# Kernel optimization log

Hardware: AMD Instinct MI355X
Metric: run time of the kernel (lower is better)

## Reference

```python
import jax, jax.numpy as jnp
import numpy as np

EPS = 1e-12  # F.normalize eps


def setup_inputs() -> dict:
    key = jax.random.key(0)
    ks = jax.random.split(key, 6)
    B, T, D = 8, 4096, 1024
    L, K, CD = 8, 1024, 16
    return {
        "z_e": jax.random.normal(ks[0], (B, T, D), jnp.float32),
        "Wd": jax.random.normal(ks[1], (L, CD, D), jnp.float32) * 0.02,
        "bd": jnp.zeros((L, CD), jnp.float32),
        "cb": jax.random.normal(ks[2], (L, K, CD), jnp.float32) * 0.02,
        "Wu": jax.random.normal(ks[3], (L, D, CD), jnp.float32) * 0.02,
        "bu": jnp.zeros((L, D), jnp.float32),
    }


def _l2norm(x):
    return x / jnp.maximum(jnp.linalg.norm(x, axis=-1, keepdims=True), EPS)


def reference(z_e, Wd, bd, cb, Wu, bu):
    """z_e: (B,T,D). Returns (z_q_concat, codes, commitment_loss, codebook_loss, entropy_loss)."""
    B, T, D = z_e.shape
    L, K, CD = cb.shape
    sg = jax.lax.stop_gradient
    residual = z_e
    zq_list, codes_list = [], []
    commit = jnp.asarray(0.0, z_e.dtype)
    cbl = jnp.asarray(0.0, z_e.dtype)
    for i in range(L):
        # proj_down: Linear(D -> CD), weight (CD, D)
        z_i = jnp.einsum('btd,cd->btc', residual, Wd[i]) + bd[i]  # (B,T,CD)
        flat = z_i.reshape(-1, CD)                                 # (N,CD)
        cb_i = cb[i]                                               # (K,CD)
        # L2-normalized lookup; argmin of euclidean cdist == argmin of squared dist
        zn, cbn = _l2norm(flat), _l2norm(cb_i)
        d2 = (jnp.sum(zn * zn, -1, keepdims=True)
              - 2.0 * (zn @ cbn.T)
              + jnp.sum(cbn * cbn, -1))                            # (N,K)
        codes = jnp.argmin(d2, axis=-1)                            # (N,)
        z_q = cb_i[codes].reshape(B, T, CD)                        # gather from RAW codebook
        commit = commit + jnp.mean((z_i - sg(z_q)) ** 2)
        cbl = cbl + jnp.mean((z_q - sg(z_i)) ** 2)
        zq_list.append(z_i + sg(z_q - z_i))                        # straight-through
        # residual update uses detached z_q; proj_up weight (D, CD)
        residual = residual - (jnp.einsum('btc,dc->btd', sg(z_q), Wu[i]) + bu[i])
        codes_list.append(codes.reshape(B, T))
    z_q_concat = jnp.concatenate(zq_list, axis=-1)                 # (B,T,L*CD)
    codes_all = jnp.stack(codes_list, axis=-1)                     # (B,T,L)
    entropy_loss = jnp.asarray(0.0, z_e.dtype)                     # entropy_loss_weight == 0
    return z_q_concat, codes_all, commit, cbl, entropy_loss
```

## Files before the change

### kernel.cpp

```cpp
#include <hip/hip_runtime.h>
#include <math.h>


#define TAU 3e-4f

#define WS_WACC   0
#define WS_HV64   64
#define WS_G64    2048
#define WS_CBN64  133120
#define WS_CBF    1247232
#define WS_G32    1902592
#define WS_HV32   1968128
#define WS_BF     1968640
#define BF_LO_OFF 131072

typedef __attribute__((ext_vector_type(8))) short short8v;
typedef __attribute__((ext_vector_type(4))) float f32x4;

__device__ __forceinline__ unsigned short bf16_rne(float x) {
    unsigned u = __float_as_uint(x);
    u += 0x7FFFu + ((u >> 16) & 1u);
    return (unsigned short)(u >> 16);
}
__device__ __forceinline__ float bf16_to_f32(unsigned short h) {
    return __uint_as_float(((unsigned)h) << 16);
}

__global__ void __launch_bounds__(256) rvq_prep(
    const float* __restrict__ cb, const float* __restrict__ Wd,
    const float* __restrict__ Wu, const float* __restrict__ bd,
    const float* __restrict__ bu,
    double* __restrict__ cbn64, unsigned short* __restrict__ cbf,
    unsigned short* __restrict__ Bf,
    double* __restrict__ G64, float* __restrict__ G32,
    double* __restrict__ hv64, float* __restrict__ hv32,
    double* __restrict__ wacc)
{
    __shared__ double sm2[1200];
    float* smf = (float*)sm2;
    const int b = blockIdx.x, t = threadIdx.x;
    if (b < 32) {
        const int idx = b * 256 + t;
        const float* cp = cb + (size_t)idx * 16;
        double v[16]; double n = 0.0;
#pragma unroll
        for (int c = 0; c < 16; ++c) { v[c] = (double)cp[c]; n = fma(v[c], v[c], n); }
        const double iv = 1.0 / fmax(sqrt(n), 1e-12);
        double* r64 = cbn64 + (size_t)idx * 17;
        unsigned short* cf = cbf + (size_t)idx * 32;
        double c2 = 0.0;
#pragma unroll
        for (int c = 0; c < 16; ++c) {
            const double x = v[c] * iv;
            c2 = fma(x, x, c2);
            r64[c] = x;
            const float xf = (float)x;
            const unsigned short hh = bf16_rne(xf);
            cf[c] = hh;
            cf[16 + c] = bf16_rne(xf - bf16_to_f32(hh));
        }
        r64[16] = c2;
    } else if (b < 96) {
        const int u = (b - 32) * 4 + (t >> 6);
        const int lane = t & 63;
        const int ks = u >> 3, ctg = u & 7;
        const int ic = ctg * 16 + (lane & 15);
        const int kb = ks * 32 + (lane >> 4) * 8;
        const float* wp = Wd + (size_t)ic * 1024 + kb;
        const float4 w0 = *(const float4*)wp;
        const float4 w1 = *(const float4*)(wp + 4);
        const float wv[8] = {w0.x, w0.y, w0.z, w0.w, w1.x, w1.y, w1.z, w1.w};
        unsigned short* dst = Bf + ((size_t)(ks * 8 + ctg) * 64 + lane) * 8;
#pragma unroll
        for (int i = 0; i < 8; ++i) {
            const unsigned short hh = bf16_rne(wv[i]);
            dst[i] = hh;
            dst[BF_LO_OFF + i] = bf16_rne(wv[i] - bf16_to_f32(hh));
        }
    } else if (b < 160) {
        const int j = (b - 96) >> 3, i = (b - 96) & 7;
        if (j >= i) return;
        float* Aus = smf;
        float* Bds = smf + 1280;
        const int a = t >> 4, bb = t & 15;
        double s = 0.0;
        for (int ch = 0; ch < 16; ++ch) {
            __syncthreads();
            {
                const int dd = t >> 2, a4 = (t & 3) * 4;
                const float4 v = *(const float4*)(Wu + (size_t)j * 16384
                                  + (size_t)(ch * 64 + dd) * 16 + a4);
                *(float4*)&Aus[dd * 20 + a4] = v;
                const int br = t >> 4, d4 = (t & 15) * 4;
                const float4 w = *(const float4*)(Wd + (size_t)i * 16384
                                  + (size_t)br * 1024 + ch * 64 + d4);
                *(float4*)&Bds[br * 68 + d4] = w;
            }
            __syncthreads();
#pragma unroll
            for (int dd = 0; dd < 64; ++dd)
                s = fma((double)Aus[dd * 20 + a], (double)Bds[bb * 68 + dd], s);
        }
        G64[(size_t)(j * 8 + i) * 256 + t] = s;
        G32[(size_t)(j * 8 + i) * 256 + t] = (float)s;
    } else if (b < 168) {
        const int i = b - 160;
        const int dq = t >> 4, bb = t & 15;
        const float* wp = Wd + (size_t)i * 16384 + (size_t)bb * 1024 + dq * 64;
        const float* bup = bu + dq * 64;
        double s = 0.0;
        for (int dd = 0; dd < 64; ++dd) {
            double sb = 0.0;
            for (int j = 0; j < i; ++j) sb += (double)bup[j * 1024 + dd];
            s = fma(sb, (double)wp[dd], s);
        }
        sm2[dq * 20 + bb] = s;
        __syncthreads();
        if (t < 16) {
            double s2 = 0.0;
#pragma unroll
            for (int q = 0; q < 16; ++q) s2 += sm2[q * 20 + t];
            const double h = (double)bd[i * 16 + t] - s2;
            hv64[i * 16 + t] = h; hv32[i * 16 + t] = (float)h;
        }
    } else {
        if (t == 0) wacc[0] = 0.0;
    }
}

__global__ void __launch_bounds__(256, 4) rvq_main(
    const float* __restrict__ z_e, const float* __restrict__ Wd,
    const float* __restrict__ cb,
    const unsigned short* __restrict__ Bf, const float* __restrict__ hv32,
    const double* __restrict__ hv64,
    const unsigned short* __restrict__ cbf, const double* __restrict__ cbn64,
    const float* __restrict__ G32, const double* __restrict__ G64,
    double* __restrict__ wacc,
    float* __restrict__ out0, float* __restrict__ out1)
{
    __shared__ __attribute__((aligned(16))) double stag_d[896];
    __shared__ float ybuf[32 * 132];
    __shared__ float candd[128], candd2[128];
    __shared__ int   candk[128];
    __shared__ float zqs[32 * 17];
    __shared__ int   bkhist[256];
    __shared__ int   bks[32], flist[32];
    __shared__ int   flagcnt;
    float* stag = reinterpret_cast<float*>(stag_d);

    const int t = threadIdx.x;
    const int tok0g = blockIdx.x * 32;
    const int wq = t >> 6, lane = t & 63;
    const int blk = lane >> 4, col = lane & 15, kh = blk & 1;
    const bool lolane = blk >= 2;

    {
        const int Ch = wq >> 1, Tt = wq & 1;
        const float* zrow = z_e + (size_t)(tok0g + Tt * 16 + col) * 1024 + blk * 8;
        const unsigned short* bfh = Bf + ((size_t)(Ch * 4) * 64 + lane) * 8;
        f32x4 acc[4];
#pragma unroll
        for (int ct = 0; ct < 4; ++ct) acc[ct] = (f32x4){0.f, 0.f, 0.f, 0.f};

#pragma unroll 2
        for (int ks = 0; ks < 32; ++ks) {
            const float4 a0 = *(const float4*)(zrow + ks * 32);
            const float4 a1 = *(const float4*)(zrow + ks * 32 + 4);
            const float av[8] = {a0.x, a0.y, a0.z, a0.w, a1.x, a1.y, a1.z, a1.w};
            short8v ah, al;
#pragma unroll
            for (int i = 0; i < 8; ++i) {
                const unsigned short hh = bf16_rne(av[i]);
                ah[i] = (short)hh;
                al[i] = (short)bf16_rne(av[i] - bf16_to_f32(hh));
            }
            const unsigned short* bp = bfh + (size_t)ks * 4096;
#pragma unroll
            for (int ct = 0; ct < 4; ++ct) {
                const short8v bh = *(const short8v*)(bp + ct * 512);
                const short8v bl = *(const short8v*)(bp + BF_LO_OFF + ct * 512);
                acc[ct] = __builtin_amdgcn_mfma_f32_16x16x32_bf16(ah, bh, acc[ct], 0, 0, 0);
                acc[ct] = __builtin_amdgcn_mfma_f32_16x16x32_bf16(ah, bl, acc[ct], 0, 0, 0);
                acc[ct] = __builtin_amdgcn_mfma_f32_16x16x32_bf16(al, bh, acc[ct], 0, 0, 0);
            }
        }
#pragma unroll
        for (int ct = 0; ct < 4; ++ct) {
            const float hvv = hv32[Ch * 64 + ct * 16 + col];
#pragma unroll
            for (int r = 0; r < 4; ++r)
                ybuf[(Tt * 16 + blk * 4 + r) * 132 + Ch * 64 + ct * 16 + col]
                    = acc[ct][r] + hvv;
        }
    }

    double lacc = 0.0;
    const int q = wq;
#pragma unroll 1
    for (int l = 0; l < 8; ++l) {
        __syncthreads();

        short8v af[2];
#pragma unroll
        for (int h = 0; h < 2; ++h) {
            const float* yp = &ybuf[(h * 16 + col) * 132 + l * 16 + kh * 8];
            const float4 y0 = *(const float4*)yp;
            const float4 y1 = *(const float4*)(yp + 4);
            const float yv[8] = {y0.x, y0.y, y0.z, y0.w, y1.x, y1.y, y1.z, y1.w};
            float p = 0.f;
#pragma unroll
            for (int i = 0; i < 8; ++i) p = fmaf(yv[i], yv[i], p);
            const float n2 = p + __shfl_xor(p, 16);
            const float iv = 1.0f / fmaxf(sqrtf(n2), 1e-12f);
#pragma unroll
            for (int i = 0; i < 8; ++i) {
                const float x = -2.f * (yv[i] * iv);
                const unsigned short hh = bf16_rne(x);
                af[h][i] = (short)(lolane ? bf16_rne(x - bf16_to_f32(hh)) : hh);
            }
        }

        float bs[2][4], bs2[2][4]; int bk[2][4];
#pragma unroll
        for (int h = 0; h < 2; ++h)
#pragma unroll
            for (int r = 0; r < 4; ++r) { bs[h][r] = 1e30f; bs2[h][r] = 1e30f; bk[h][r] = -1; }
        const unsigned short* cbp = cbf + ((size_t)(l * 1024 + q * 256 + col)) * 32;
        const unsigned short* p1 = cbp + kh * 8;
        const unsigned short* p2 = cbp + 16 + kh * 8;
#pragma unroll 2
        for (int tile = 0; tile < 16; ++tile) {
            const short8v b1 = *(const short8v*)(p1 + tile * 512);
            short8v b2 = {};
            if (!lolane) b2 = *(const short8v*)(p2 + tile * 512);
            f32x4 aa[2];
            aa[0] = (f32x4){0.f, 0.f, 0.f, 0.f};
            aa[0] = __builtin_amdgcn_mfma_f32_16x16x32_bf16(af[0], b1, aa[0], 0, 0, 0);
            aa[0] = __builtin_amdgcn_mfma_f32_16x16x32_bf16(af[0], b2, aa[0], 0, 0, 0);
            aa[1] = (f32x4){0.f, 0.f, 0.f, 0.f};
            aa[1] = __builtin_amdgcn_mfma_f32_16x16x32_bf16(af[1], b1, aa[1], 0, 0, 0);
            aa[1] = __builtin_amdgcn_mfma_f32_16x16x32_bf16(af[1], b2, aa[1], 0, 0, 0);
            const int k = q * 256 + tile * 16 + col;
#pragma unroll
            for (int h = 0; h < 2; ++h)
#pragma unroll
                for (int r = 0; r < 4; ++r) {
                    const float s = aa[h][r];
                    const bool wn = s < bs[h][r];
                    bs2[h][r] = wn ? bs[h][r] : fminf(bs2[h][r], s);
                    bk[h][r]  = wn ? k : bk[h][r];
                    bs[h][r]  = wn ? s : bs[h][r];
                }
        }

#pragma unroll
        for (int m = 1; m <= 8; m <<= 1)
#pragma unroll
            for (int h = 0; h < 2; ++h)
#pragma unroll
                for (int r = 0; r < 4; ++r) {
                    const float ob = __shfl_xor(bs[h][r], m);
                    const float os = __shfl_xor(bs2[h][r], m);
                    const int   ok = __shfl_xor(bk[h][r], m);
                    const bool wn = (ob < bs[h][r]) || (ob == bs[h][r] && ok < bk[h][r]);
                    const float loser = wn ? bs[h][r] : ob;
                    bs2[h][r] = fminf(fminf(bs2[h][r], os), loser);
                    bs[h][r]  = wn ? ob : bs[h][r];
                    bk[h][r]  = wn ? ok : bk[h][r];
                }
        if (t == 0) flagcnt = 0;
        if (col == 0) {
#pragma unroll
            for (int h = 0; h < 2; ++h)
#pragma unroll
                for (int r = 0; r < 4; ++r) {
                    const int tok = h * 16 + blk * 4 + r;
                    candd [q * 32 + tok] = bs[h][r];
                    candd2[q * 32 + tok] = bs2[h][r];
                    candk [q * 32 + tok] = bk[h][r];
                }
        }
        __syncthreads();
        if (t < 32) {
            float best = 1e30f, sec = 1e30f; int bkk = -1;
#pragma unroll
            for (int c = 0; c < 4; ++c) {
                const float d  = candd [c * 32 + t];
                const float d2 = candd2[c * 32 + t];
                const int   k  = candk [c * 32 + t];
                const bool wn = (d < best) || (d == best && k < bkk);
                const float nw = fminf(sec, fminf(best, d2));
                const float nl = fminf(sec, d);
                sec  = wn ? nw : nl;
                bkk  = wn ? k : bkk;
                best = wn ? d : best;
            }
            bks[t] = bkk;
            const float* yr = &ybuf[t * 132 + l * 16];
            float n2 = 0.f;
#pragma unroll
            for (int c = 0; c < 16; ++c) n2 = fmaf(yr[c], yr[c], n2);
            if ((sec - best < TAU) || (n2 < 1e-3f)) {
                const int p = atomicAdd(&flagcnt, 1); flist[p] = t;
            }
        }
        __syncthreads();

        const int nf = flagcnt;
#pragma unroll 1
        for (int f = 0; f < nf; ++f) {
            const int tok = flist[f];
            double* rpd = stag_d;
            {
                const int c = t & 15, ch = t >> 4;
                const float* gz = z_e + (size_t)(tok0g + tok) * 1024 + ch * 64;
                const float* wp = Wd + ((size_t)l * 16 + c) * 1024 + ch * 64;
                double pd = 0.0;
                for (int dd = 0; dd < 64; ++dd)
                    pd = fma((double)gz[dd], (double)wp[dd], pd);
                rpd[c * 16 + ch] = pd;
            }
            __syncthreads();
            if (t < 16) {
                double y = hv64[l * 16 + t];
#pragma unroll
                for (int ch = 0; ch < 16; ++ch) y += rpd[t * 16 + ch];
                for (int j = 0; j < l; ++j) {
                    const int bkj = bkhist[tok * 8 + j];
                    const float* qv = cb + ((size_t)j * 1024 + bkj) * 16;
                    const double* gp = G64 + (size_t)(j * 8 + l) * 256 + t;
                    double s = 0.0;
#pragma unroll
                    for (int a = 0; a < 16; ++a)
                        s = fma((double)qv[a], gp[a * 16], s);
                    y -= s;
                }
                rpd[256 + t] = y;
            }
            __syncthreads();
            if (t == 0) {
                double n2 = 0.0;
#pragma unroll
                for (int c = 0; c < 16; ++c) n2 = fma(rpd[256 + c], rpd[256 + c], n2);
                const double iv = 1.0 / fmax(sqrt(n2), 1e-12);
#pragma unroll
                for (int c = 0; c < 16; ++c) rpd[272 + c] = rpd[256 + c] * iv;
            }
            __syncthreads();
            {
                double bd_ = 1e300; int bk_ = -1;
#pragma unroll
                for (int qq = 0; qq < 4; ++qq) {
                    const int k = qq * 256 + t;
                    const double* row = cbn64 + (size_t)(l * 1024 + k) * 17;
                    double dot = 0.0;
#pragma unroll
                    for (int c = 0; c < 16; ++c) dot = fma(row[c], rpd[272 + c], dot);
                    const double s = fma(-2.0, dot, row[16]);
                    if (s < bd_) { bd_ = s; bk_ = k; }
                }
                rpd[288 + t] = bd_;
                ((int*)&rpd[544])[t] = bk_;
            }
            __syncthreads();
            if (t == 0) {
                double bd_ = 1e300; int bk_ = -1;
                for (int i = 0; i < 256; ++i) {
                    const double d = rpd[288 + i];
                    const int k = ((int*)&rpd[544])[i];
                    if (d < bd_ || (d == bd_ && k < bk_)) { bd_ = d; bk_ = k; }
                }
                bks[tok] = bk_;
            }
            __syncthreads();
        }

        if (t < 32) {
            const int bk_ = bks[t];
            bkhist[t * 8 + l] = bk_;
            const float4* qp = (const float4*)(cb + ((size_t)l * 1024 + bk_) * 16);
            const float4 q0 = qp[0], q1 = qp[1], q2 = qp[2], q3 = qp[3];
            float* op = out0 + (size_t)(tok0g + t) * 128 + l * 16;
            ((float4*)op)[0] = q0; ((float4*)op)[1] = q1;
            ((float4*)op)[2] = q2; ((float4*)op)[3] = q3;
            out1[(size_t)(tok0g + t) * 8 + l] = (float)bk_;
            const float qf[16] = {q0.x,q0.y,q0.z,q0.w, q1.x,q1.y,q1.z,q1.w,
                                  q2.x,q2.y,q2.z,q2.w, q3.x,q3.y,q3.z,q3.w};
#pragma unroll
            for (int a = 0; a < 16; ++a) zqs[t * 17 + a] = qf[a];
            const float* yr = &ybuf[t * 132 + l * 16];
#pragma unroll
            for (int c = 0; c < 16; ++c) {
                const float d = yr[c] - qf[c];
                lacc += (double)d * (double)d;
            }
        }
        __syncthreads();

        if (l < 7) {
            {
                const int total = (7 - l) * 256;
                for (int idx = t; idx < total; idx += 256) {
                    const int ii = l + 1 + (idx >> 8);
                    stag[idx] = G32[(size_t)(l * 8 + ii) * 256 + (idx & 255)];
                }
            }
            __syncthreads();
            const int part = t >> 5, tok = t & 31;
            const int ii = l + 1 + part;
            if (ii < 8) {
                float zql[16];
#pragma unroll
                for (int a = 0; a < 16; ++a) zql[a] = zqs[tok * 17 + a];
                const float* gb = &stag[part * 256];
                float corr[16];
#pragma unroll
                for (int x = 0; x < 16; ++x) corr[x] = 0.f;
#pragma unroll
                for (int a = 0; a < 16; ++a) {
                    const float4 g0 = *(const float4*)&gb[a * 16];
                    const float4 g1 = *(const float4*)&gb[a * 16 + 4];
                    const float4 g2 = *(const float4*)&gb[a * 16 + 8];
                    const float4 g3 = *(const float4*)&gb[a * 16 + 12];
                    const float za = zql[a];
                    corr[0]  = fmaf(za, g0.x, corr[0]);  corr[1]  = fmaf(za, g0.y, corr[1]);
                    corr[2]  = fmaf(za, g0.z, corr[2]);  corr[3]  = fmaf(za, g0.w, corr[3]);
                    corr[4]  = fmaf(za, g1.x, corr[4]);  corr[5]  = fmaf(za, g1.y, corr[5]);
                    corr[6]  = fmaf(za, g1.z, corr[6]);  corr[7]  = fmaf(za, g1.w, corr[7]);
                    corr[8]  = fmaf(za, g2.x, corr[8]);  corr[9]  = fmaf(za, g2.y, corr[9]);
                    corr[10] = fmaf(za, g2.z, corr[10]); corr[11] = fmaf(za, g2.w, corr[11]);
                    corr[12] = fmaf(za, g3.x, corr[12]); corr[13] = fmaf(za, g3.y, corr[13]);
                    corr[14] = fmaf(za, g3.z, corr[14]); corr[15] = fmaf(za, g3.w, corr[15]);
                }
                float* yr = &ybuf[tok * 132 + ii * 16];
#pragma unroll
                for (int v = 0; v < 4; ++v) {
                    float4 y4 = *(float4*)&yr[v * 4];
                    y4.x -= corr[v * 4 + 0]; y4.y -= corr[v * 4 + 1];
                    y4.z -= corr[v * 4 + 2]; y4.w -= corr[v * 4 + 3];
                    *(float4*)&yr[v * 4] = y4;
                }
            }
        }
    }

    if (t < 64) {
#pragma unroll
        for (int off = 32; off > 0; off >>= 1) lacc += __shfl_down(lacc, off);
        if (t == 0) atomicAdd(wacc, lacc);
    }
}

__global__ void __launch_bounds__(64) rvq_fin(const double* __restrict__ wacc,
                                              float* __restrict__ lossp) {
    if (threadIdx.x == 0) {
        const float v = (float)(wacc[0] * (1.0 / 524288.0));
        lossp[0] = v; lossp[1] = v; lossp[2] = 0.0f;
    }
}

extern "C" void kernel_launch(void* const* d_in, const int* in_sizes, int n_in,
                              void* d_out, int out_size, void* d_ws, size_t ws_size,
                              hipStream_t stream) {
    (void)in_sizes; (void)n_in; (void)ws_size;
    const float* z_e = (const float*)d_in[0];
    const float* Wd  = (const float*)d_in[1];
    const float* bd  = (const float*)d_in[2];
    const float* cb  = (const float*)d_in[3];
    const float* Wu  = (const float*)d_in[4];
    const float* bu  = (const float*)d_in[5];

    float* out0  = (float*)d_out;
    float* out1  = out0 + (size_t)8 * 4096 * 128;
    float* lossp = out0 + (size_t)out_size - 3;

    char* ws = (char*)d_ws;
    double* wacc  = (double*)(ws + WS_WACC);
    double* hv64  = (double*)(ws + WS_HV64);
    double* G64   = (double*)(ws + WS_G64);
    double* cbn64 = (double*)(ws + WS_CBN64);
    unsigned short* cbf = (unsigned short*)(ws + WS_CBF);
    float*  G32   = (float*) (ws + WS_G32);
    float*  hv32  = (float*) (ws + WS_HV32);
    unsigned short* Bf = (unsigned short*)(ws + WS_BF);

    rvq_prep<<<169, 256, 0, stream>>>(cb, Wd, Wu, bd, bu, cbn64, cbf, Bf,
                                      G64, G32, hv64, hv32, wacc);
    rvq_main<<<1024, 256, 0, stream>>>(z_e, Wd, cb, Bf, hv32, hv64,
                                       cbf, cbn64, G32, G64, wacc, out0, out1);
    rvq_fin<<<1, 64, 0, stream>>>(wacc, lossp);
}
```

Before: 622.5 us.

## Keep projected residuals in MFMA registers and apply inter-level corrections via MFMA

The projected activations now stay in MFMA accumulator registers instead of a 32x132 LDS buffer. Each level's residual correction (z_q times the Gram matrix G) runs as split bf16 MFMAs, with G pre-packed in hi/lo bf16 in the prep kernel, replacing the LDS-staged scalar FMA loop and its extra barriers. Output writes are deferred to one coalesced pass at the end, and the bf16 hi/lo splits use packed v_cvt_pk_bf16_f32 conversions. This cuts LDS traffic and syncs and may raise occupancy, but the correction now carries bf16-split precision and is missing the lo×lo term.

```diff
diff --git a/kernel.cpp b/kernel.cpp
--- a/kernel.cpp
+++ b/kernel.cpp
@@ -9,13 +9,14 @@
 #define WS_G64    2048
 #define WS_CBN64  133120
 #define WS_CBF    1247232
-#define WS_G32    1902592
-#define WS_HV32   1968128
-#define WS_BF     1968640
+#define WS_GF     1771520
+#define WS_HV32   1837056
+#define WS_BF     1837568
 #define BF_LO_OFF 131072
 
 typedef __attribute__((ext_vector_type(8))) short short8v;
 typedef __attribute__((ext_vector_type(4))) float f32x4;
+typedef __attribute__((ext_vector_type(4))) unsigned int uint4v;
 
 __device__ __forceinline__ unsigned short bf16_rne(float x) {
     unsigned u = __float_as_uint(x);
@@ -24,6 +25,32 @@
 }
 __device__ __forceinline__ float bf16_to_f32(unsigned short h) {
     return __uint_as_float(((unsigned)h) << 16);
+}
+__device__ __forceinline__ unsigned cvt_pk_bf16(float lo, float hi) {
+    unsigned r;
+    asm("v_cvt_pk_bf16_f32 %0, %1, %2" : "=v"(r) : "v"(lo), "v"(hi));
+    return r;
+}
+__device__ __forceinline__ void cvt_hilo8(const float* v, short8v& hi, short8v& lo) {
+    uint4v uh, ul;
+#pragma unroll
+    for (int i = 0; i < 4; ++i) {
+        const unsigned u = cvt_pk_bf16(v[2 * i], v[2 * i + 1]);
+        uh[i] = u;
+        const float r0 = v[2 * i]     - __uint_as_float(u << 16);
+        const float r1 = v[2 * i + 1] - __uint_as_float(u & 0xFFFF0000u);
+        ul[i] = cvt_pk_bf16(r0, r1);
+    }
+    hi = __builtin_bit_cast(short8v, uh);
+    lo = __builtin_bit_cast(short8v, ul);
+}
+__device__ __forceinline__ short8v vsel8(bool c, short8v a, short8v b) {
+    uint4v ua = __builtin_bit_cast(uint4v, a);
+    uint4v ub = __builtin_bit_cast(uint4v, b);
+    uint4v r;
+#pragma unroll
+    for (int i = 0; i < 4; ++i) r[i] = c ? ua[i] : ub[i];
+    return __builtin_bit_cast(short8v, r);
 }
 
 __global__ void __launch_bounds__(256) rvq_prep(
@@ -31,8 +58,8 @@
     const float* __restrict__ Wu, const float* __restrict__ bd,
     const float* __restrict__ bu,
     double* __restrict__ cbn64, unsigned short* __restrict__ cbf,
-    unsigned short* __restrict__ Bf,
-    double* __restrict__ G64, float* __restrict__ G32,
+    unsigned short* __restrict__ Bf, unsigned short* __restrict__ Gf,
+    double* __restrict__ G64,
     double* __restrict__ hv64, float* __restrict__ hv32,
     double* __restrict__ wacc)
 {
@@ -102,7 +129,12 @@
                 s = fma((double)Aus[dd * 20 + a], (double)Bds[bb * 68 + dd], s);
         }
         G64[(size_t)(j * 8 + i) * 256 + t] = s;
-        G32[(size_t)(j * 8 + i) * 256 + t] = (float)s;
+        const float gs = (float)s;
+        const unsigned short gh = bf16_rne(gs);
+        const unsigned short gl = bf16_rne(gs - bf16_to_f32(gh));
+        unsigned short* gf = Gf + (size_t)(j * 8 + i) * 512;
+        gf[(((a >> 3) * 16 + bb) * 8) + (a & 7)] = gh;
+        gf[((((a >> 3) + 2) * 16 + bb) * 8) + (a & 7)] = gl;
     } else if (b < 168) {
         const int i = b - 160;
         const int dq = t >> 4, bb = t & 15;
@@ -134,46 +166,38 @@
     const unsigned short* __restrict__ Bf, const float* __restrict__ hv32,
     const double* __restrict__ hv64,
     const unsigned short* __restrict__ cbf, const double* __restrict__ cbn64,
-    const float* __restrict__ G32, const double* __restrict__ G64,
+    const unsigned short* __restrict__ Gf, const double* __restrict__ G64,
     double* __restrict__ wacc,
     float* __restrict__ out0, float* __restrict__ out1)
 {
-    __shared__ __attribute__((aligned(16))) double stag_d[896];
-    __shared__ float ybuf[32 * 132];
+    __shared__ __attribute__((aligned(16))) double stag_d[672];
+    __shared__ float ynow[32 * 20];
     __shared__ float candd[128], candd2[128];
     __shared__ int   candk[128];
-    __shared__ float zqs[32 * 17];
     __shared__ int   bkhist[256];
     __shared__ int   bks[32], flist[32];
     __shared__ int   flagcnt;
-    float* stag = reinterpret_cast<float*>(stag_d);
 
     const int t = threadIdx.x;
     const int tok0g = blockIdx.x * 32;
     const int wq = t >> 6, lane = t & 63;
     const int blk = lane >> 4, col = lane & 15, kh = blk & 1;
     const bool lolane = blk >= 2;
-
+    const int Tt = wq & 1, Ch = wq >> 1;
+
+    f32x4 acc[4];
+#pragma unroll
+    for (int ct = 0; ct < 4; ++ct) acc[ct] = (f32x4){0.f, 0.f, 0.f, 0.f};
     {
-        const int Ch = wq >> 1, Tt = wq & 1;
         const float* zrow = z_e + (size_t)(tok0g + Tt * 16 + col) * 1024 + blk * 8;
         const unsigned short* bfh = Bf + ((size_t)(Ch * 4) * 64 + lane) * 8;
-        f32x4 acc[4];
-#pragma unroll
-        for (int ct = 0; ct < 4; ++ct) acc[ct] = (f32x4){0.f, 0.f, 0.f, 0.f};
-
 #pragma unroll 2
         for (int ks = 0; ks < 32; ++ks) {
             const float4 a0 = *(const float4*)(zrow + ks * 32);
             const float4 a1 = *(const float4*)(zrow + ks * 32 + 4);
             const float av[8] = {a0.x, a0.y, a0.z, a0.w, a1.x, a1.y, a1.z, a1.w};
             short8v ah, al;
-#pragma unroll
-            for (int i = 0; i < 8; ++i) {
-                const unsigned short hh = bf16_rne(av[i]);
-                ah[i] = (short)hh;
-                al[i] = (short)bf16_rne(av[i] - bf16_to_f32(hh));
-            }
+            cvt_hilo8(av, ah, al);
             const unsigned short* bp = bfh + (size_t)ks * 4096;
 #pragma unroll
             for (int ct = 0; ct < 4; ++ct) {
@@ -188,22 +212,25 @@
         for (int ct = 0; ct < 4; ++ct) {
             const float hvv = hv32[Ch * 64 + ct * 16 + col];
 #pragma unroll
-            for (int r = 0; r < 4; ++r)
-                ybuf[(Tt * 16 + blk * 4 + r) * 132 + Ch * 64 + ct * 16 + col]
-                    = acc[ct][r] + hvv;
+            for (int r = 0; r < 4; ++r) acc[ct][r] += hvv;
         }
     }
 
     double lacc = 0.0;
-    const int q = wq;
 #pragma unroll 1
     for (int l = 0; l < 8; ++l) {
+        if (Ch == (l >> 2)) {
+            const int ct = l & 3;
+#pragma unroll
+            for (int r = 0; r < 4; ++r)
+                ynow[(Tt * 16 + blk * 4 + r) * 20 + col] = acc[ct][r];
+        }
         __syncthreads();
 
         short8v af[2];
 #pragma unroll
         for (int h = 0; h < 2; ++h) {
-            const float* yp = &ybuf[(h * 16 + col) * 132 + l * 16 + kh * 8];
+            const float* yp = &ynow[(h * 16 + col) * 20 + kh * 8];
             const float4 y0 = *(const float4*)yp;
             const float4 y1 = *(const float4*)(yp + 4);
             const float yv[8] = {y0.x, y0.y, y0.z, y0.w, y1.x, y1.y, y1.z, y1.w};
@@ -212,12 +239,12 @@
             for (int i = 0; i < 8; ++i) p = fmaf(yv[i], yv[i], p);
             const float n2 = p + __shfl_xor(p, 16);
             const float iv = 1.0f / fmaxf(sqrtf(n2), 1e-12f);
-#pragma unroll
-            for (int i = 0; i < 8; ++i) {
-                const float x = -2.f * (yv[i] * iv);
-                const unsigned short hh = bf16_rne(x);
-                af[h][i] = (short)(lolane ? bf16_rne(x - bf16_to_f32(hh)) : hh);
-            }
+            float xv[8];
+#pragma unroll
+            for (int i = 0; i < 8; ++i) xv[i] = -2.f * (yv[i] * iv);
+            short8v hi8, lo8;
+            cvt_hilo8(xv, hi8, lo8);
+            af[h] = vsel8(lolane, lo8, hi8);
         }
 
         float bs[2][4], bs2[2][4]; int bk[2][4];
@@ -225,7 +252,7 @@
         for (int h = 0; h < 2; ++h)
 #pragma unroll
             for (int r = 0; r < 4; ++r) { bs[h][r] = 1e30f; bs2[h][r] = 1e30f; bk[h][r] = -1; }
-        const unsigned short* cbp = cbf + ((size_t)(l * 1024 + q * 256 + col)) * 32;
+        const unsigned short* cbp = cbf + ((size_t)(l * 1024 + wq * 256 + col)) * 32;
         const unsigned short* p1 = cbp + kh * 8;
         const unsigned short* p2 = cbp + 16 + kh * 8;
 #pragma unroll 2
@@ -240,7 +267,7 @@
             aa[1] = (f32x4){0.f, 0.f, 0.f, 0.f};
             aa[1] = __builtin_amdgcn_mfma_f32_16x16x32_bf16(af[1], b1, aa[1], 0, 0, 0);
             aa[1] = __builtin_amdgcn_mfma_f32_16x16x32_bf16(af[1], b2, aa[1], 0, 0, 0);
-            const int k = q * 256 + tile * 16 + col;
+            const int k = wq * 256 + tile * 16 + col;
 #pragma unroll
             for (int h = 0; h < 2; ++h)
 #pragma unroll
@@ -275,9 +302,9 @@
 #pragma unroll
                 for (int r = 0; r < 4; ++r) {
                     const int tok = h * 16 + blk * 4 + r;
-                    candd [q * 32 + tok] = bs[h][r];
-                    candd2[q * 32 + tok] = bs2[h][r];
-                    candk [q * 32 + tok] = bk[h][r];
+                    candd [wq * 32 + tok] = bs[h][r];
+                    candd2[wq * 32 + tok] = bs2[h][r];
+                    candk [wq * 32 + tok] = bk[h][r];
                 }
         }
         __syncthreads();
@@ -296,10 +323,12 @@
                 best = wn ? d : best;
             }
             bks[t] = bkk;
-            const float* yr = &ybuf[t * 132 + l * 16];
             float n2 = 0.f;
 #pragma unroll
-            for (int c = 0; c < 16; ++c) n2 = fmaf(yr[c], yr[c], n2);
+            for (int c = 0; c < 16; ++c) {
+                const float yv = ynow[t * 20 + c];
+                n2 = fmaf(yv, yv, n2);
+            }
             if ((sec - best < TAU) || (n2 < 1e-3f)) {
                 const int p = atomicAdd(&flagcnt, 1); flist[p] = t;
             }
@@ -380,68 +409,50 @@
             bkhist[t * 8 + l] = bk_;
             const float4* qp = (const float4*)(cb + ((size_t)l * 1024 + bk_) * 16);
             const float4 q0 = qp[0], q1 = qp[1], q2 = qp[2], q3 = qp[3];
-            float* op = out0 + (size_t)(tok0g + t) * 128 + l * 16;
-            ((float4*)op)[0] = q0; ((float4*)op)[1] = q1;
-            ((float4*)op)[2] = q2; ((float4*)op)[3] = q3;
-            out1[(size_t)(tok0g + t) * 8 + l] = (float)bk_;
             const float qf[16] = {q0.x,q0.y,q0.z,q0.w, q1.x,q1.y,q1.z,q1.w,
                                   q2.x,q2.y,q2.z,q2.w, q3.x,q3.y,q3.z,q3.w};
 #pragma unroll
-            for (int a = 0; a < 16; ++a) zqs[t * 17 + a] = qf[a];
-            const float* yr = &ybuf[t * 132 + l * 16];
-#pragma unroll
             for (int c = 0; c < 16; ++c) {
-                const float d = yr[c] - qf[c];
+                const float d = ynow[t * 20 + c] - qf[c];
                 lacc += (double)d * (double)d;
             }
         }
+
+        if (l < 7) {
+            const int code = bks[Tt * 16 + col];
+            const float* qrow = cb + ((size_t)l * 1024 + code) * 16 + kh * 8;
+            const float4 q0 = *(const float4*)qrow;
+            const float4 q1 = *(const float4*)(qrow + 4);
+            const float xv[8] = {-q0.x, -q0.y, -q0.z, -q0.w,
+                                 -q1.x, -q1.y, -q1.z, -q1.w};
+            short8v zh8, zl8;
+            cvt_hilo8(xv, zh8, zl8);
+            const short8v zero = {};
+            const short8v a1 = zh8;
+            const short8v a2 = vsel8(lolane, zero, zl8);
+#pragma unroll
+            for (int ct = 0; ct < 4; ++ct) {
+                const int ii = Ch * 4 + ct;
+                if (ii > l) {
+                    const short8v b1 = *(const short8v*)(Gf +
+                        ((size_t)(l * 8 + ii)) * 512 + lane * 8);
+                    const short8v b2 = vsel8(lolane, zero, b1);
+                    acc[ct] = __builtin_amdgcn_mfma_f32_16x16x32_bf16(a1, b1, acc[ct], 0, 0, 0);
+                    acc[ct] = __builtin_amdgcn_mfma_f32_16x16x32_bf16(a2, b2, acc[ct], 0, 0, 0);
+                }
+            }
+        }
         __syncthreads();
-
-        if (l < 7) {
-            {
-                const int total = (7 - l) * 256;
-                for (int idx = t; idx < total; idx += 256) {
-                    const int ii = l + 1 + (idx >> 8);
-                    stag[idx] = G32[(size_t)(l * 8 + ii) * 256 + (idx & 255)];
-                }
-            }
-            __syncthreads();
-            const int part = t >> 5, tok = t & 31;
-            const int ii = l + 1 + part;
-            if (ii < 8) {
-                float zql[16];
-#pragma unroll
-                for (int a = 0; a < 16; ++a) zql[a] = zqs[tok * 17 + a];
-                const float* gb = &stag[part * 256];
-                float corr[16];
-#pragma unroll
-                for (int x = 0; x < 16; ++x) corr[x] = 0.f;
-#pragma unroll
-                for (int a = 0; a < 16; ++a) {
-                    const float4 g0 = *(const float4*)&gb[a * 16];
-                    const float4 g1 = *(const float4*)&gb[a * 16 + 4];
-                    const float4 g2 = *(const float4*)&gb[a * 16 + 8];
-                    const float4 g3 = *(const float4*)&gb[a * 16 + 12];
-                    const float za = zql[a];
-                    corr[0]  = fmaf(za, g0.x, corr[0]);  corr[1]  = fmaf(za, g0.y, corr[1]);
-                    corr[2]  = fmaf(za, g0.z, corr[2]);  corr[3]  = fmaf(za, g0.w, corr[3]);
-                    corr[4]  = fmaf(za, g1.x, corr[4]);  corr[5]  = fmaf(za, g1.y, corr[5]);
-                    corr[6]  = fmaf(za, g1.z, corr[6]);  corr[7]  = fmaf(za, g1.w, corr[7]);
-                    corr[8]  = fmaf(za, g2.x, corr[8]);  corr[9]  = fmaf(za, g2.y, corr[9]);
-                    corr[10] = fmaf(za, g2.z, corr[10]); corr[11] = fmaf(za, g2.w, corr[11]);
-                    corr[12] = fmaf(za, g3.x, corr[12]); corr[13] = fmaf(za, g3.y, corr[13]);
-                    corr[14] = fmaf(za, g3.z, corr[14]); corr[15] = fmaf(za, g3.w, corr[15]);
-                }
-                float* yr = &ybuf[tok * 132 + ii * 16];
-#pragma unroll
-                for (int v = 0; v < 4; ++v) {
-                    float4 y4 = *(float4*)&yr[v * 4];
-                    y4.x -= corr[v * 4 + 0]; y4.y -= corr[v * 4 + 1];
-                    y4.z -= corr[v * 4 + 2]; y4.w -= corr[v * 4 + 3];
-                    *(float4*)&yr[v * 4] = y4;
-                }
-            }
-        }
+    }
+
+    {
+        const int tok = t >> 3, li = t & 7;
+        const int code = bkhist[tok * 8 + li];
+        const float4* qp = (const float4*)(cb + ((size_t)li * 1024 + code) * 16);
+        float* op = out0 + (size_t)(tok0g + tok) * 128 + li * 16;
+        ((float4*)op)[0] = qp[0]; ((float4*)op)[1] = qp[1];
+        ((float4*)op)[2] = qp[2]; ((float4*)op)[3] = qp[3];
+        out1[(size_t)(tok0g + tok) * 8 + li] = (float)code;
     }
 
     if (t < 64) {
@@ -480,13 +491,13 @@
     double* G64   = (double*)(ws + WS_G64);
     double* cbn64 = (double*)(ws + WS_CBN64);
     unsigned short* cbf = (unsigned short*)(ws + WS_CBF);
-    float*  G32   = (float*) (ws + WS_G32);
+    unsigned short* Gf  = (unsigned short*)(ws + WS_GF);
     float*  hv32  = (float*) (ws + WS_HV32);
-    unsigned short* Bf = (unsigned short*)(ws + WS_BF);
-
-    rvq_prep<<<169, 256, 0, stream>>>(cb, Wd, Wu, bd, bu, cbn64, cbf, Bf,
-                                      G64, G32, hv64, hv32, wacc);
+    unsigned short* Bf  = (unsigned short*)(ws + WS_BF);
+
+    rvq_prep<<<169, 256, 0, stream>>>(cb, Wd, Wu, bd, bu, cbn64, cbf, Bf, Gf,
+                                      G64, hv64, hv32, wacc);
     rvq_main<<<1024, 256, 0, stream>>>(z_e, Wd, cb, Bf, hv32, hv64,
-                                       cbf, cbn64, G32, G64, wacc, out0, out1);
+                                       cbf, cbn64, Gf, G64, wacc, out0, out1);
     rvq_fin<<<1, 64, 0, stream>>>(wacc, lossp);
 }
```

Result: slower. 644.9 us (+3.6%).
